# Performance work log

Measured on AMD Instinct MI355X. Metric: run time of the kernel, lower is better.

The kernel has to match this reference:

```python
import jax, jax.numpy as jnp
import numpy as np

B, T, D, N = 2, 2048, 1024, 16
DT_RANK = 64  # ceil(D / 16)


def setup_inputs() -> dict:
    key = jax.random.key(0)
    ks = jax.random.split(key, 8)
    x = jax.random.normal(ks[0], (B, T, D), dtype=jnp.float32)
    # Linear weights stored as (out, in) like torch; applied as x @ W.T
    W_B = jax.random.normal(ks[1], (N, D), dtype=jnp.float32) / np.sqrt(D)
    W_C = jax.random.normal(ks[2], (N, D), dtype=jnp.float32) / np.sqrt(D)
    W_dt1 = jax.random.normal(ks[3], (DT_RANK, D), dtype=jnp.float32) / np.sqrt(D)
    W_dt2 = jax.random.normal(ks[4], (D, DT_RANK), dtype=jnp.float32) / np.sqrt(DT_RANK)
    # dt bias init: inverse-softplus of dt sampled log-uniform in [dt_min, dt_max]
    dt_min, dt_max = 1e-3, 1e-1
    u = jax.random.uniform(ks[5], (D,), dtype=jnp.float32)
    dt_init = jnp.clip(jnp.exp(u * (np.log(dt_max) - np.log(dt_min)) + np.log(dt_min)), 1e-4, None)
    b_dt2 = dt_init + jnp.log(-jnp.expm1(-dt_init))
    # log_A: per original non-HiPPO path, A in (0.5, 1.0), broadcast to (D, N)
    a = jax.random.uniform(ks[6], (N,), dtype=jnp.float32) * 0.5 + 0.5
    log_A = jnp.broadcast_to(jnp.log(a)[None, :], (D, N)).copy()
    D_skip = jnp.ones((D,), dtype=jnp.float32)
    return {"x": x, "W_B": W_B, "W_C": W_C, "W_dt1": W_dt1,
            "W_dt2": W_dt2, "b_dt2": b_dt2, "log_A": log_A, "D_skip": D_skip}


def _selective_scan(A_bar, B_bar, C):
    # A_bar, B_bar: (B, T, D, N); C: (B, T, N) -> y: (B, T, D)
    def step(h, inputs):
        a_t, b_t, c_t = inputs  # (B,D,N), (B,D,N), (B,N)
        h = a_t * h + b_t
        y_t = jnp.einsum('bdn,bn->bd', h, c_t)
        return h, y_t

    h0 = jnp.zeros(A_bar.shape[:1] + A_bar.shape[2:], dtype=A_bar.dtype)  # (B,D,N)
    xs = (jnp.moveaxis(A_bar, 1, 0), jnp.moveaxis(B_bar, 1, 0), jnp.moveaxis(C, 1, 0))
    _, ys = jax.lax.scan(step, h0, xs)  # ys: (T, B, D)
    return jnp.moveaxis(ys, 0, 1)


def reference(x, W_B, W_C, W_dt1, W_dt2, b_dt2, log_A, D_skip):
    # Projections
    B_t = jnp.einsum('btd,nd->btn', x, W_B)          # (B,T,N)
    C_t = jnp.einsum('btd,nd->btn', x, W_C)          # (B,T,N)
    dt_raw = jnp.einsum('btr,dr->btd', jnp.einsum('btd,rd->btr', x, W_dt1), W_dt2) + b_dt2
    dt = jax.nn.softplus(dt_raw)                     # (B,T,D)
    A = -jnp.exp(log_A)                              # (D,N), negative
    # Discretization
    A_bar = jnp.exp(dt[..., None] * A[None, None])   # (B,T,D,N)
    dB = (A_bar - 1.0) / (A[None, None] + 1e-8)
    B_bar = dB * x[..., None] * B_t[:, :, None, :]   # (B,T,D,N)
    y = _selective_scan(A_bar, B_bar, C_t)           # (B,T,D)
    return y + D_skip * x
```

## Files before the change

kernel.cpp:

```cpp
#include <hip/hip_runtime.h>
#include <hip/hip_bf16.h>

#define BB 2
#define TT 2048
#define DD 1024
#define NN 16
#define RR 64
#define MM (BB*TT)
#define KDIM DD
#define CHUNK 32
#define NCHUNK (TT/CHUNK)
#define KSPLIT 8

#define BT_OFF 0
#define CT_OFF 65536
#define R1_OFF 131072
#define DT_OFF 393216
#define P_OFF  4587520
#define S_OFF  6684672
#define H_OFF  8781824
#define PP_OFF 10878976

#define LOG2E 1.4426950408889634f

#if __has_builtin(__builtin_amdgcn_exp2f)
#define EXP2(x) __builtin_amdgcn_exp2f(x)
#else
#define EXP2(x) exp2f(x)
#endif

__device__ __forceinline__ float softplus_f(float z) {
    return fmaxf(z, 0.0f) + log1pf(expf(-fabsf(z)));
}

__global__ __launch_bounds__(256) void k_proj96(
    const float* __restrict__ x, const float* __restrict__ W_B,
    const float* __restrict__ W_C, const float* __restrict__ W_dt1,
    float* __restrict__ Pp)
{
    __shared__ float xs[16][68];
    __shared__ float wsT[16][97];

    const int tid = threadIdx.x;
    const int r0 = blockIdx.x * 64;
    const int kbase = blockIdx.y * (KDIM / KSPLIT);
    const int tx = tid & 15;
    const int ty = tid >> 4;

    float acc[4][6];
    #pragma unroll
    for (int i = 0; i < 4; i++)
        #pragma unroll
        for (int j = 0; j < 6; j++) acc[i][j] = 0.0f;

    for (int kc = 0; kc < KDIM / KSPLIT; kc += 16) {
        {
            const int row = tid >> 2;
            const int kq = (tid & 3) * 4;
            float4 v = *(const float4*)(x + (size_t)(r0 + row) * KDIM + kbase + kc + kq);
            xs[kq + 0][row] = v.x; xs[kq + 1][row] = v.y;
            xs[kq + 2][row] = v.z; xs[kq + 3][row] = v.w;
        }
        #pragma unroll
        for (int i = 0; i < 6; i++) {
            const int idx = i * 256 + tid;
            const int c = idx >> 4;
            const int kk = idx & 15;
            const float* wrow; int cc;
            if (c < 16)      { wrow = W_B;   cc = c; }
            else if (c < 32) { wrow = W_C;   cc = c - 16; }
            else             { wrow = W_dt1; cc = c - 32; }
            wsT[kk][c] = wrow[(size_t)cc * KDIM + kbase + kc + kk];
        }
        __syncthreads();
        #pragma unroll
        for (int kk = 0; kk < 16; kk++) {
            const float a0 = xs[kk][ty * 4 + 0];
            const float a1 = xs[kk][ty * 4 + 1];
            const float a2 = xs[kk][ty * 4 + 2];
            const float a3 = xs[kk][ty * 4 + 3];
            #pragma unroll
            for (int j = 0; j < 6; j++) {
                const float b = wsT[kk][tx + j * 16];
                acc[0][j] = fmaf(a0, b, acc[0][j]);
                acc[1][j] = fmaf(a1, b, acc[1][j]);
                acc[2][j] = fmaf(a2, b, acc[2][j]);
                acc[3][j] = fmaf(a3, b, acc[3][j]);
            }
        }
        __syncthreads();
    }

    float* out = Pp + (size_t)blockIdx.y * (MM * 96);
    #pragma unroll
    for (int i = 0; i < 4; i++) {
        const int r = r0 + ty * 4 + i;
        #pragma unroll
        for (int j = 0; j < 6; j++)
            out[(size_t)r * 96 + tx + j * 16] = acc[i][j];
    }
}

__global__ __launch_bounds__(256) void k_reduce96(
    const float* __restrict__ Pp, const float* __restrict__ log_A,
    float* __restrict__ Bt, float* __restrict__ Ct, float* __restrict__ R1)
{
    const int gid = blockIdx.x * 256 + threadIdx.x;
    const int e0 = gid * 4;
    float4 s = *(const float4*)(Pp + e0);
    #pragma unroll
    for (int p = 1; p < KSPLIT; p++) {
        const float4 v = *(const float4*)(Pp + (size_t)p * MM * 96 + e0);
        s.x += v.x; s.y += v.y; s.z += v.z; s.w += v.w;
    }
    const int r = e0 / 96;
    const int c = e0 - r * 96;
    if (c < 16) {
        const float4 lgj = *(const float4*)(log_A + c);
        s.x *= 1.0f / (-__expf(lgj.x) + 1e-8f);
        s.y *= 1.0f / (-__expf(lgj.y) + 1e-8f);
        s.z *= 1.0f / (-__expf(lgj.z) + 1e-8f);
        s.w *= 1.0f / (-__expf(lgj.w) + 1e-8f);
        *(float4*)(Bt + (size_t)r * NN + c) = s;
    } else if (c < 32) {
        *(float4*)(Ct + (size_t)r * NN + (c - 16)) = s;
    } else {
        *(float4*)(R1 + (size_t)r * RR + (c - 32)) = s;
    }
}

__global__ __launch_bounds__(256, 4) void k_dtproj(
    const float* __restrict__ R1, const float* __restrict__ W_dt2,
    const float* __restrict__ b_dt2, float* __restrict__ dt)
{
    __shared__ float r1s[64][68];
    __shared__ float wsT[64][68];

    const int tid = threadIdx.x;
    const int r0 = blockIdx.x * 64;
    const int d0 = blockIdx.y * 64;

    #pragma unroll
    for (int i = 0; i < 4; i++) {
        const int f = tid + i * 256;
        const int row = f >> 4;
        const int kq = (f & 15) * 4;
        *(float4*)&r1s[row][kq] = *(const float4*)(R1 + (size_t)(r0 + row) * RR + kq);
    }
    {
        const int dl = tid >> 2;
        const int kq0 = (tid & 3) * 16;
        const float* src = W_dt2 + (size_t)(d0 + dl) * RR + kq0;
        #pragma unroll
        for (int j = 0; j < 16; j += 4) {
            const float4 v = *(const float4*)(src + j);
            wsT[kq0 + j + 0][dl] = v.x;
            wsT[kq0 + j + 1][dl] = v.y;
            wsT[kq0 + j + 2][dl] = v.z;
            wsT[kq0 + j + 3][dl] = v.w;
        }
    }
    __syncthreads();

    const int cg = tid & 15;
    const int rg = tid >> 4;

    float4 acc[4];
    #pragma unroll
    for (int i = 0; i < 4; i++) acc[i] = make_float4(0.f, 0.f, 0.f, 0.f);

    #pragma unroll
    for (int k4 = 0; k4 < 16; k4++) {
        float r1a[4][4];
        #pragma unroll
        for (int i = 0; i < 4; i++) {
            const float4 v = *(const float4*)&r1s[rg * 4 + i][k4 * 4];
            r1a[i][0] = v.x; r1a[i][1] = v.y; r1a[i][2] = v.z; r1a[i][3] = v.w;
        }
        #pragma unroll
        for (int kk = 0; kk < 4; kk++) {
            const float4 w = *(const float4*)&wsT[k4 * 4 + kk][cg * 4];
            #pragma unroll
            for (int i = 0; i < 4; i++) {
                const float a = r1a[i][kk];
                acc[i].x = fmaf(a, w.x, acc[i].x);
                acc[i].y = fmaf(a, w.y, acc[i].y);
                acc[i].z = fmaf(a, w.z, acc[i].z);
                acc[i].w = fmaf(a, w.w, acc[i].w);
            }
        }
    }

    const float4 bias = *(const float4*)(b_dt2 + d0 + cg * 4);
    #pragma unroll
    for (int i = 0; i < 4; i++) {
        const int row = r0 + rg * 4 + i;
        float4 o;
        o.x = softplus_f(acc[i].x + bias.x);
        o.y = softplus_f(acc[i].y + bias.y);
        o.z = softplus_f(acc[i].z + bias.z);
        o.w = softplus_f(acc[i].w + bias.w);
        *(float4*)(dt + (size_t)row * DD + d0 + cg * 4) = o;
    }
}

__global__ __launch_bounds__(256, 4) void k_scan1(
    const float* __restrict__ x, const float* __restrict__ dt,
    const float* __restrict__ Bt, const float* __restrict__ log_A,
    float* __restrict__ P, float* __restrict__ Sg)
{
    __shared__ float bt_s[CHUNK][NN];

    const int tid = threadIdx.x;
    const int ng = tid & 1;
    const int dl = tid >> 1;
    const int d = blockIdx.x * 128 + dl;
    const int c = blockIdx.y;
    const int b = blockIdx.z;
    const int n0 = ng * 8;
    const int base = b * TT + c * CHUNK;

    if (tid < CHUNK * NN / 4) {
        const int t = tid >> 2;
        const int jc = (tid & 3) * 4;
        *(float4*)&bt_s[t][jc] = *(const float4*)(Bt + (size_t)(base + t) * NN + jc);
    }

    const float* gdt = dt + (size_t)base * DD + d;
    const float* gx  = x  + (size_t)base * DD + d;
    float dv[CHUNK], xv[CHUNK];
    #pragma unroll
    for (int t = 0; t < CHUNK; t++) {
        dv[t] = gdt[(size_t)t * DD];
        xv[t] = gx[(size_t)t * DD];
    }

    float A2[8];
    #pragma unroll
    for (int q = 0; q < 2; q++) {
        const float4 lg = *(const float4*)(log_A + d * NN + n0 + q * 4);
        A2[q * 4 + 0] = -__expf(lg.x) * LOG2E;
        A2[q * 4 + 1] = -__expf(lg.y) * LOG2E;
        A2[q * 4 + 2] = -__expf(lg.z) * LOG2E;
        A2[q * 4 + 3] = -__expf(lg.w) * LOG2E;
    }

    __syncthreads();

    float s[8];
    #pragma unroll
    for (int n = 0; n < 8; n++) s[n] = 0.0f;
    float dtsum = 0.0f;

    #pragma unroll
    for (int t = 0; t < CHUNK; t++) {
        const float dtv = dv[t];
        const float xvv = xv[t];
        dtsum += dtv;
        #pragma unroll
        for (int q = 0; q < 2; q++) {
            const float4 bt4 = *(const float4*)&bt_s[t][n0 + q * 4];
            const float a0 = EXP2(dtv * A2[q * 4 + 0]);
            const float a1 = EXP2(dtv * A2[q * 4 + 1]);
            const float a2 = EXP2(dtv * A2[q * 4 + 2]);
            const float a3 = EXP2(dtv * A2[q * 4 + 3]);
            const float u0 = xvv * bt4.x;
            const float u1 = xvv * bt4.y;
            const float u2 = xvv * bt4.z;
            const float u3 = xvv * bt4.w;
            s[q * 4 + 0] = fmaf(a0, s[q * 4 + 0] + u0, -u0);
            s[q * 4 + 1] = fmaf(a1, s[q * 4 + 1] + u1, -u1);
            s[q * 4 + 2] = fmaf(a2, s[q * 4 + 2] + u2, -u2);
            s[q * 4 + 3] = fmaf(a3, s[q * 4 + 3] + u3, -u3);
        }
    }

    const size_t o = ((size_t)(c * BB + b) * DD + d) * NN + n0;
    #pragma unroll
    for (int q = 0; q < 2; q++) {
        *(float4*)(P + o + q * 4) = make_float4(
            EXP2(A2[q * 4 + 0] * dtsum), EXP2(A2[q * 4 + 1] * dtsum),
            EXP2(A2[q * 4 + 2] * dtsum), EXP2(A2[q * 4 + 3] * dtsum));
        *(float4*)(Sg + o + q * 4) = make_float4(
            s[q * 4 + 0], s[q * 4 + 1], s[q * 4 + 2], s[q * 4 + 3]);
    }
}

__global__ __launch_bounds__(256) void k_comb(
    const float* __restrict__ P, const float* __restrict__ Sg,
    float* __restrict__ Hs)
{
    const int flat = blockIdx.x * 256 + threadIdx.x;
    float h = 0.0f;
    #pragma unroll 8
    for (int c = 0; c < NCHUNK; c++) {
        const size_t idx = (size_t)c * (BB * DD * NN) + flat;
        Hs[idx] = h;
        h = fmaf(P[idx], h, Sg[idx]);
    }
}

__global__ __launch_bounds__(256, 4) void k_scan2(
    const float* __restrict__ x, const float* __restrict__ dt,
    const float* __restrict__ Bt, const float* __restrict__ Ct,
    const float* __restrict__ log_A, const float* __restrict__ D_skip,
    const float* __restrict__ Hs, float* __restrict__ y)
{
    __shared__ float bt_s[CHUNK][NN];
    __shared__ float ct_s[CHUNK][NN];

    const int tid = threadIdx.x;
    const int ng = tid & 1;
    const int dl = tid >> 1;
    const int d = blockIdx.x * 128 + dl;
    const int c = blockIdx.y;
    const int b = blockIdx.z;
    const int n0 = ng * 8;
    const int base = b * TT + c * CHUNK;

    if (tid < 128) {
        const int t = tid >> 2;
        const int jc = (tid & 3) * 4;
        *(float4*)&bt_s[t][jc] = *(const float4*)(Bt + (size_t)(base + t) * NN + jc);
    } else {
        const int t2 = (tid - 128) >> 2;
        const int jc = (tid & 3) * 4;
        *(float4*)&ct_s[t2][jc] = *(const float4*)(Ct + (size_t)(base + t2) * NN + jc);
    }

    const float* gdt = dt + (size_t)base * DD + d;
    const float* gx  = x  + (size_t)base * DD + d;
    float dv[CHUNK], xv[CHUNK];
    #pragma unroll
    for (int t = 0; t < CHUNK; t++) {
        dv[t] = gdt[(size_t)t * DD];
        xv[t] = gx[(size_t)t * DD];
    }

    float A2[8];
    #pragma unroll
    for (int q = 0; q < 2; q++) {
        const float4 lg = *(const float4*)(log_A + d * NN + n0 + q * 4);
        A2[q * 4 + 0] = -__expf(lg.x) * LOG2E;
        A2[q * 4 + 1] = -__expf(lg.y) * LOG2E;
        A2[q * 4 + 2] = -__expf(lg.z) * LOG2E;
        A2[q * 4 + 3] = -__expf(lg.w) * LOG2E;
    }
    const float dsk = D_skip[d];

    float h[8];
    {
        const size_t hoff = (size_t)c * (BB * DD * NN) + (size_t)b * (DD * NN)
                          + (size_t)d * NN + n0;
        #pragma unroll
        for (int q = 0; q < 2; q++) {
            const float4 hv = *(const float4*)(Hs + hoff + q * 4);
            h[q * 4 + 0] = hv.x; h[q * 4 + 1] = hv.y;
            h[q * 4 + 2] = hv.z; h[q * 4 + 3] = hv.w;
        }
    }

    __syncthreads();

    float* yp = y + (size_t)base * DD + d;

    #pragma unroll
    for (int t = 0; t < CHUNK; t++) {
        const float dtv = dv[t];
        const float xvv = xv[t];
        float part = 0.0f;
        #pragma unroll
        for (int q = 0; q < 2; q++) {
            const float4 bt4 = *(const float4*)&bt_s[t][n0 + q * 4];
            const float4 ct4 = *(const float4*)&ct_s[t][n0 + q * 4];
            const float a0 = EXP2(dtv * A2[q * 4 + 0]);
            const float a1 = EXP2(dtv * A2[q * 4 + 1]);
            const float a2 = EXP2(dtv * A2[q * 4 + 2]);
            const float a3 = EXP2(dtv * A2[q * 4 + 3]);
            const float u0 = xvv * bt4.x;
            const float u1 = xvv * bt4.y;
            const float u2 = xvv * bt4.z;
            const float u3 = xvv * bt4.w;
            h[q * 4 + 0] = fmaf(a0, h[q * 4 + 0] + u0, -u0);
            h[q * 4 + 1] = fmaf(a1, h[q * 4 + 1] + u1, -u1);
            h[q * 4 + 2] = fmaf(a2, h[q * 4 + 2] + u2, -u2);
            h[q * 4 + 3] = fmaf(a3, h[q * 4 + 3] + u3, -u3);
            part = fmaf(h[q * 4 + 0], ct4.x, part);
            part = fmaf(h[q * 4 + 1], ct4.y, part);
            part = fmaf(h[q * 4 + 2], ct4.z, part);
            part = fmaf(h[q * 4 + 3], ct4.w, part);
        }
        part += __shfl_xor(part, 1);
        if (ng == 0) yp[(size_t)t * DD] = fmaf(dsk, xvv, part);
    }
}

extern "C" void kernel_launch(void* const* d_in, const int* in_sizes, int n_in,
                              void* d_out, int out_size, void* d_ws, size_t ws_size,
                              hipStream_t stream)
{
    const float* x      = (const float*)d_in[0];
    const float* W_B    = (const float*)d_in[1];
    const float* W_C    = (const float*)d_in[2];
    const float* W_dt1  = (const float*)d_in[3];
    const float* W_dt2  = (const float*)d_in[4];
    const float* b_dt2  = (const float*)d_in[5];
    const float* log_A  = (const float*)d_in[6];
    const float* D_skip = (const float*)d_in[7];
    float* y = (float*)d_out;

    float* ws = (float*)d_ws;
    float* Bt = ws + BT_OFF;
    float* Ct = ws + CT_OFF;
    float* R1 = ws + R1_OFF;
    float* dt = ws + DT_OFF;
    float* P  = ws + P_OFF;
    float* S  = ws + S_OFF;
    float* Hs = ws + H_OFF;
    float* Pp = ws + PP_OFF;

    k_proj96<<<dim3(MM / 64, KSPLIT), 256, 0, stream>>>(x, W_B, W_C, W_dt1, Pp);
    k_reduce96<<<dim3(MM * 96 / 4 / 256), 256, 0, stream>>>(Pp, log_A, Bt, Ct, R1);
    k_dtproj<<<dim3(MM / 64, DD / 64), 256, 0, stream>>>(R1, W_dt2, b_dt2, dt);
    k_scan1<<<dim3(DD / 128, NCHUNK, BB), 256, 0, stream>>>(x, dt, Bt, log_A, P, S);
    k_comb<<<dim3(BB * DD * NN / 256), 256, 0, stream>>>(P, S, Hs);
    k_scan2<<<dim3(DD / 128, NCHUNK, BB), 256, 0, stream>>>(x, dt, Bt, Ct, log_A, D_skip, Hs, y);
}
```

Before: 162.8 us.

## Rewrite dt projection as register-resident weights with broadcast R1 rows

The dt up-projection kernel stops staging R1 and transposed W_dt2 tiles in shared memory. Each thread now holds one output column's 64 weights in registers and loops over 16 rows, reading R1 rows that are uniform across the block. The aim is to drop LDS traffic and the block barrier. In exchange it uses far more registers per thread, re-reads R1 from cache for every block along D, and writes outputs one float per thread instead of float4.

Measured after the change: 168.8 us. +3.7%, slower.

```diff
diff --git a/kernel.cpp b/kernel.cpp
--- a/kernel.cpp
+++ b/kernel.cpp
@@ -133,74 +133,36 @@
     const float* __restrict__ R1, const float* __restrict__ W_dt2,
     const float* __restrict__ b_dt2, float* __restrict__ dt)
 {
-    __shared__ float r1s[64][68];
-    __shared__ float wsT[64][68];
-
     const int tid = threadIdx.x;
-    const int r0 = blockIdx.x * 64;
-    const int d0 = blockIdx.y * 64;
-
-    #pragma unroll
-    for (int i = 0; i < 4; i++) {
-        const int f = tid + i * 256;
-        const int row = f >> 4;
-        const int kq = (f & 15) * 4;
-        *(float4*)&r1s[row][kq] = *(const float4*)(R1 + (size_t)(r0 + row) * RR + kq);
-    }
-    {
-        const int dl = tid >> 2;
-        const int kq0 = (tid & 3) * 16;
-        const float* src = W_dt2 + (size_t)(d0 + dl) * RR + kq0;
-        #pragma unroll
-        for (int j = 0; j < 16; j += 4) {
-            const float4 v = *(const float4*)(src + j);
-            wsT[kq0 + j + 0][dl] = v.x;
-            wsT[kq0 + j + 1][dl] = v.y;
-            wsT[kq0 + j + 2][dl] = v.z;
-            wsT[kq0 + j + 3][dl] = v.w;
-        }
-    }
-    __syncthreads();
-
-    const int cg = tid & 15;
-    const int rg = tid >> 4;
-
-    float4 acc[4];
-    #pragma unroll
-    for (int i = 0; i < 4; i++) acc[i] = make_float4(0.f, 0.f, 0.f, 0.f);
-
-    #pragma unroll
-    for (int k4 = 0; k4 < 16; k4++) {
-        float r1a[4][4];
-        #pragma unroll
-        for (int i = 0; i < 4; i++) {
-            const float4 v = *(const float4*)&r1s[rg * 4 + i][k4 * 4];
-            r1a[i][0] = v.x; r1a[i][1] = v.y; r1a[i][2] = v.z; r1a[i][3] = v.w;
-        }
-        #pragma unroll
-        for (int kk = 0; kk < 4; kk++) {
-            const float4 w = *(const float4*)&wsT[k4 * 4 + kk][cg * 4];
-            #pragma unroll
-            for (int i = 0; i < 4; i++) {
-                const float a = r1a[i][kk];
-                acc[i].x = fmaf(a, w.x, acc[i].x);
-                acc[i].y = fmaf(a, w.y, acc[i].y);
-                acc[i].z = fmaf(a, w.z, acc[i].z);
-                acc[i].w = fmaf(a, w.w, acc[i].w);
-            }
-        }
-    }
-
-    const float4 bias = *(const float4*)(b_dt2 + d0 + cg * 4);
-    #pragma unroll
-    for (int i = 0; i < 4; i++) {
-        const int row = r0 + rg * 4 + i;
-        float4 o;
-        o.x = softplus_f(acc[i].x + bias.x);
-        o.y = softplus_f(acc[i].y + bias.y);
-        o.z = softplus_f(acc[i].z + bias.z);
-        o.w = softplus_f(acc[i].w + bias.w);
-        *(float4*)(dt + (size_t)row * DD + d0 + cg * 4) = o;
+    const int r0 = blockIdx.x * 16;
+    const int d  = blockIdx.y * 256 + tid;
+
+    float4 w4[16];
+    #pragma unroll
+    for (int q = 0; q < 16; q++)
+        w4[q] = *(const float4*)(W_dt2 + (size_t)d * RR + q * 4);
+    const float bias = b_dt2[d];
+
+    #pragma unroll
+    for (int r = 0; r < 16; r++) {
+        const float* r1p = R1 + (size_t)(r0 + r) * RR;
+        float pa0 = bias, pa1 = 0.f, pa2 = 0.f, pa3 = 0.f;
+        #pragma unroll
+        for (int q = 0; q < 16; q += 4) {
+            const float4 a0 = *(const float4*)(r1p + (q + 0) * 4);
+            const float4 a1 = *(const float4*)(r1p + (q + 1) * 4);
+            const float4 a2 = *(const float4*)(r1p + (q + 2) * 4);
+            const float4 a3 = *(const float4*)(r1p + (q + 3) * 4);
+            pa0 = fmaf(a0.x, w4[q + 0].x, pa0); pa0 = fmaf(a0.y, w4[q + 0].y, pa0);
+            pa0 = fmaf(a0.z, w4[q + 0].z, pa0); pa0 = fmaf(a0.w, w4[q + 0].w, pa0);
+            pa1 = fmaf(a1.x, w4[q + 1].x, pa1); pa1 = fmaf(a1.y, w4[q + 1].y, pa1);
+            pa1 = fmaf(a1.z, w4[q + 1].z, pa1); pa1 = fmaf(a1.w, w4[q + 1].w, pa1);
+            pa2 = fmaf(a2.x, w4[q + 2].x, pa2); pa2 = fmaf(a2.y, w4[q + 2].y, pa2);
+            pa2 = fmaf(a2.z, w4[q + 2].z, pa2); pa2 = fmaf(a2.w, w4[q + 2].w, pa2);
+            pa3 = fmaf(a3.x, w4[q + 3].x, pa3); pa3 = fmaf(a3.y, w4[q + 3].y, pa3);
+            pa3 = fmaf(a3.z, w4[q + 3].z, pa3); pa3 = fmaf(a3.w, w4[q + 3].w, pa3);
+        }
+        dt[(size_t)(r0 + r) * DD + d] = softplus_f((pa0 + pa1) + (pa2 + pa3));
     }
 }
 
@@ -421,7 +383,7 @@
 
     k_proj96<<<dim3(MM / 64, KSPLIT), 256, 0, stream>>>(x, W_B, W_C, W_dt1, Pp);
     k_reduce96<<<dim3(MM * 96 / 4 / 256), 256, 0, stream>>>(Pp, log_A, Bt, Ct, R1);
-    k_dtproj<<<dim3(MM / 64, DD / 64), 256, 0, stream>>>(R1, W_dt2, b_dt2, dt);
+    k_dtproj<<<dim3(MM / 16, DD / 256), 256, 0, stream>>>(R1, W_dt2, b_dt2, dt);
     k_scan1<<<dim3(DD / 128, NCHUNK, BB), 256, 0, stream>>>(x, dt, Bt, log_A, P, S);
     k_comb<<<dim3(BB * DD * NN / 256), 256, 0, stream>>>(P, S, Hs);
     k_scan2<<<dim3(DD / 128, NCHUNK, BB), 256, 0, stream>>>(x, dt, Bt, Ct, log_A, D_skip, Hs, y);
```
